# Kernel optimization log

Hardware: AMD Instinct MI355X
Metric: run time of the kernel (lower is better)

Reference implementation:

```python
import math
import jax, jax.numpy as jnp
import numpy as np
from jax import lax

# Block_mamba(dim=192): x = x + Mamba(LN1(x)); x = x + EinFFT(LN2(x), H, W)
DIM = 192
D_STATE = 64
D_CONV = 4
EXPAND = 2
D_INNER = EXPAND * DIM          # 384
DT_RANK = math.ceil(DIM / 16)   # 12
NUM_BLOCKS = 4                  # EinFFT hardcoded
BLOCK_SIZE = DIM // NUM_BLOCKS  # 48
LAMBDA = 0.01                   # softshrink threshold


def setup_inputs() -> dict:
    key = jax.random.key(0)
    ks = jax.random.split(key, 20)
    B, N, C = 4, 1024, DIM
    s = 0.02
    x = jax.random.normal(ks[0], (B, N, C), jnp.float32)
    inp = {
        "x": x,
        "ln1_w": jnp.ones((C,), jnp.float32),
        "ln1_b": jnp.zeros((C,), jnp.float32),
        "in_proj_w": jax.random.normal(ks[1], (2 * D_INNER, C), jnp.float32) * s,
        "conv_w": jax.random.normal(ks[2], (D_INNER, 1, D_CONV), jnp.float32) * 0.1,
        "conv_b": jnp.zeros((D_INNER,), jnp.float32),
        "x_proj_w": jax.random.normal(ks[3], (DT_RANK + 2 * D_STATE, D_INNER), jnp.float32) * s,
        "dt_proj_w": jax.random.normal(ks[4], (D_INNER, DT_RANK), jnp.float32) * (DT_RANK ** -0.5),
        "dt_proj_b": jax.random.uniform(ks[5], (D_INNER,), jnp.float32, -4.0, -2.0),
        "A_log": jnp.log(jnp.broadcast_to(jnp.arange(1, D_STATE + 1, dtype=jnp.float32), (D_INNER, D_STATE))),
        "D": jnp.ones((D_INNER,), jnp.float32),
        "out_proj_w": jax.random.normal(ks[6], (C, D_INNER), jnp.float32) * s,
        "ln2_w": jnp.ones((C,), jnp.float32),
        "ln2_b": jnp.zeros((C,), jnp.float32),
        "cw1": jax.random.normal(ks[7], (2, NUM_BLOCKS, BLOCK_SIZE, BLOCK_SIZE), jnp.float32) * s,
        "cw2": jax.random.normal(ks[8], (2, NUM_BLOCKS, BLOCK_SIZE, BLOCK_SIZE), jnp.float32) * s,
        "cb1": jax.random.normal(ks[9], (2, NUM_BLOCKS, BLOCK_SIZE), jnp.float32) * s,
        "cb2": jax.random.normal(ks[10], (2, NUM_BLOCKS, BLOCK_SIZE), jnp.float32) * s,
        "H": 32,
        "W": 32,
    }
    return inp


def layer_norm(x, w, b, eps=1e-5):
    mu = jnp.mean(x, axis=-1, keepdims=True)
    var = jnp.var(x, axis=-1, keepdims=True)
    return (x - mu) * lax.rsqrt(var + eps) * w + b


def mamba(x, in_proj_w, conv_w, conv_b, x_proj_w, dt_proj_w, dt_proj_b, A_log, D):
    B, L, C = x.shape
    xz = jnp.einsum('blc,ec->ble', x, in_proj_w)          # [B,L,2*D_INNER]
    xm, z = jnp.split(xz, 2, axis=-1)                      # each [B,L,D_INNER]
    # causal depthwise conv1d (torch pads both sides then slices [:, :, :L])
    xc = lax.conv_general_dilated(
        xm.transpose(0, 2, 1), conv_w, (1,), [(D_CONV - 1, 0)],
        dimension_numbers=('NCH', 'OIH', 'NCH'), feature_group_count=D_INNER)
    xm = jax.nn.silu(xc + conv_b[None, :, None]).transpose(0, 2, 1)  # [B,L,D_INNER]
    dbc = jnp.einsum('bld,ed->ble', xm, x_proj_w)
    dt, Bm, Cm = jnp.split(dbc, [DT_RANK, DT_RANK + D_STATE], axis=-1)
    delta = jax.nn.softplus(jnp.einsum('blr,dr->bld', dt, dt_proj_w) + dt_proj_b)  # [B,L,D_INNER]
    A = -jnp.exp(A_log)                                    # [D_INNER, D_STATE]

    def step(h, inp):
        d_t, B_t, C_t, x_t = inp                           # [B,d],[B,n],[B,n],[B,d]
        dA = jnp.exp(d_t[:, :, None] * A)                  # [B,d,n]
        h = h * dA + (d_t * x_t)[:, :, None] * B_t[:, None, :]
        y = jnp.einsum('bdn,bn->bd', h, C_t)
        return h, y

    h0 = jnp.zeros((B, D_INNER, D_STATE), x.dtype)
    xs = (delta.transpose(1, 0, 2), Bm.transpose(1, 0, 2), Cm.transpose(1, 0, 2), xm.transpose(1, 0, 2))
    _, ys = lax.scan(step, h0, xs)                         # ys: [L,B,d]
    y = ys.transpose(1, 0, 2) + xm * D
    y = y * jax.nn.silu(z)
    return jnp.einsum('bld,cd->blc', y, out_proj_w_global[0])


# small trick to keep mamba signature tidy
out_proj_w_global = [None]


def einfft(x, cw1, cw2, cb1, cb2):
    B, N, C = x.shape
    xv = x.reshape(B, N, NUM_BLOCKS, BLOCK_SIZE)
    pad1 = (1 << math.ceil(math.log2(N))) - N
    pad2 = (1 << math.ceil(math.log2(NUM_BLOCKS))) - NUM_BLOCKS
    if pad1 or pad2:
        xv = jnp.pad(xv, ((0, 0), (0, pad1), (0, pad2), (0, 0)))
    X = jnp.fft.fft2(xv, axes=(1, 2), norm='ortho')
    mul = lambda t, w: jnp.einsum('Bnbd,bdk->Bnbk', t, w)
    r1 = jax.nn.relu(mul(X.real, cw1[0]) - mul(X.imag, cw1[1]) + cb1[0])
    i1 = jax.nn.relu(mul(X.real, cw1[1]) + mul(X.imag, cw1[0]) + cb1[1])
    r2 = mul(r1, cw2[0]) - mul(i1, cw2[1]) + cb2[0]
    i2 = mul(r1, cw2[1]) + mul(i1, cw2[0]) + cb2[1]
    ss = lambda v: jnp.where(v > LAMBDA, v - LAMBDA, jnp.where(v < -LAMBDA, v + LAMBDA, jnp.zeros((), v.dtype)))
    Z = ss(r2) + 1j * ss(i2)
    y = jnp.fft.ifft2(Z, axes=(1, 2), norm='ortho')[:, :N, :NUM_BLOCKS, :]
    return y.real.reshape(B, N, C)  # torch .to(real dtype) keeps real part


def reference(x, ln1_w, ln1_b, in_proj_w, conv_w, conv_b, x_proj_w, dt_proj_w, dt_proj_b,
              A_log, D, out_proj_w, ln2_w, ln2_b, cw1, cw2, cb1, cb2, H, W):
    out_proj_w_global[0] = out_proj_w
    x = x + mamba(layer_norm(x, ln1_w, ln1_b), in_proj_w, conv_w, conv_b,
                  x_proj_w, dt_proj_w, dt_proj_b, A_log, D)
    x = x + einfft(layer_norm(x, ln2_w, ln2_b), cw1, cw2, cb1, cb2)
    return x
```

## Files before the change

kernel.cpp:

```cpp
#include <hip/hip_runtime.h>
#include <math.h>

#define PI_F 3.14159265358979323846f

typedef __attribute__((ext_vector_type(8))) short short8v;
typedef __attribute__((ext_vector_type(4))) float f32x4;

__device__ __forceinline__ float lane_bcast(float v, int l) {
  return __int_as_float(__builtin_amdgcn_readlane(__float_as_int(v), l));
}

__device__ __forceinline__ unsigned short f2bf(float f) {
  unsigned u = __float_as_uint(f);
  unsigned r = u + 0x7FFFu + ((u >> 16) & 1u);
  return (unsigned short)(r >> 16);
}

__device__ __forceinline__ float wave_reduce_sum(float v) {
  v += __shfl_xor(v, 32, 64);
  v += __shfl_xor(v, 16, 64);
  v += __shfl_xor(v, 8, 64);
  v += __shfl_xor(v, 4, 64);
  v += __shfl_xor(v, 2, 64);
  v += __shfl_xor(v, 1, 64);
  return v;
}

__global__ __launch_bounds__(256) void ln_kernel(const float* __restrict__ x,
    const float* __restrict__ w, const float* __restrict__ b,
    const float* __restrict__ ipw, unsigned short* __restrict__ obf,
    unsigned short* __restrict__ wbf) {
  int row = blockIdx.x * 4 + (threadIdx.x >> 6);
  int lane = threadIdx.x & 63;
  const float* xr = x + (size_t)row * 192;
  float v0 = xr[lane], v1 = xr[lane + 64], v2 = xr[lane + 128];
  float s  = wave_reduce_sum(v0 + v1 + v2);
  float s2 = wave_reduce_sum(v0 * v0 + v1 * v1 + v2 * v2);
  float mu  = s * (1.f / 192.f);
  float var = s2 * (1.f / 192.f) - mu * mu;
  float rs  = rsqrtf(var + 1e-5f);
  unsigned short* orow = obf + (size_t)row * 192;
  orow[lane]       = f2bf((v0 - mu) * rs * w[lane]       + b[lane]);
  orow[lane + 64]  = f2bf((v1 - mu) * rs * w[lane + 64]  + b[lane + 64]);
  orow[lane + 128] = f2bf((v2 - mu) * rs * w[lane + 128] + b[lane + 128]);
  for (int i = threadIdx.x; i < 144; i += 256) {
    int idx = blockIdx.x * 144 + i;
    wbf[idx] = f2bf(ipw[idx]);
  }
}

__global__ __launch_bounds__(256) void gemm_mfma_in(
    const unsigned short* __restrict__ Abf, const unsigned short* __restrict__ Wbf,
    float* __restrict__ C) {
  int wave = threadIdx.x >> 6;
  int lane = threadIdx.x & 63;
  int m0 = blockIdx.y * 64 + wave * 16;
  int n0 = blockIdx.x * 64;
  int rw = lane & 15;
  int g  = lane >> 4;
  const unsigned short* Ap = Abf + (size_t)(m0 + rw) * 192 + g * 8;
  const unsigned short* Wp = Wbf + (size_t)(n0 + rw) * 192 + g * 8;
  f32x4 acc[4];
#pragma unroll
  for (int f = 0; f < 4; ++f) acc[f] = (f32x4){0.f, 0.f, 0.f, 0.f};
#pragma unroll
  for (int kk = 0; kk < 192; kk += 32) {
    short8v a = *(const short8v*)(Ap + kk);
#pragma unroll
    for (int f = 0; f < 4; ++f) {
      short8v bfr = *(const short8v*)(Wp + (size_t)f * 16 * 192 + kk);
      acc[f] = __builtin_amdgcn_mfma_f32_16x16x32_bf16(a, bfr, acc[f], 0, 0, 0);
    }
  }
#pragma unroll
  for (int f = 0; f < 4; ++f)
#pragma unroll
    for (int r = 0; r < 4; ++r)
      C[(size_t)(m0 + g * 4 + r) * 768 + n0 + f * 16 + rw] = acc[f][r];
}

__global__ __launch_bounds__(256) void gemm_mfma_xp(
    const unsigned short* __restrict__ Abf, const unsigned short* __restrict__ Wbf,
    float* __restrict__ C) {
  int wave = threadIdx.x >> 6;
  int lane = threadIdx.x & 63;
  int m0 = blockIdx.y * 64 + wave * 16;
  int n0 = blockIdx.x * 64;
  int rw = lane & 15;
  int g  = lane >> 4;
  const unsigned short* Ap = Abf + (size_t)(m0 + rw) * 384 + g * 8;
  f32x4 acc[4];
#pragma unroll
  for (int f = 0; f < 4; ++f) acc[f] = (f32x4){0.f, 0.f, 0.f, 0.f};
  short8v bz = {0, 0, 0, 0, 0, 0, 0, 0};
#pragma unroll
  for (int kk = 0; kk < 384; kk += 32) {
    short8v a = *(const short8v*)(Ap + kk);
#pragma unroll
    for (int f = 0; f < 4; ++f) {
      int n = n0 + f * 16 + rw;
      short8v bfr = (n < 140)
        ? *(const short8v*)(Wbf + (size_t)n * 384 + g * 8 + kk) : bz;
      acc[f] = __builtin_amdgcn_mfma_f32_16x16x32_bf16(a, bfr, acc[f], 0, 0, 0);
    }
  }
#pragma unroll
  for (int f = 0; f < 4; ++f)
#pragma unroll
    for (int r = 0; r < 4; ++r) {
      int n = n0 + f * 16 + rw;
      if (n < 140)
        C[(size_t)(m0 + g * 4 + r) * 140 + n] = acc[f][r];
    }
}

__global__ __launch_bounds__(256) void gemm_at32m(const float* __restrict__ AT,
    const unsigned short* __restrict__ Wbf, const float* __restrict__ res,
    float* __restrict__ C) {
  __shared__ unsigned As[64][17];
  int tid = threadIdx.x;
  int wave = tid >> 6, lane = tid & 63;
  int n0 = blockIdx.x * 64;
  int m0 = blockIdx.y * 64;
  int bb = m0 >> 10;
  int t0 = m0 & 1023;
  const float* Ab = AT + ((size_t)bb * 384) * 1024 + t0;
  int col = tid & 63;
  int kq  = tid >> 6;
  int rw = lane & 15, g = lane >> 4;
  f32x4 acc[4];
#pragma unroll
  for (int f = 0; f < 4; ++f) acc[f] = (f32x4){0.f, 0.f, 0.f, 0.f};
#pragma unroll
  for (int kk = 0; kk < 384; kk += 32) {
#pragma unroll
    for (int p = 0; p < 4; ++p) {
      int k2 = kq + p * 4;
      int k = kk + k2 * 2;
      float f0 = Ab[(size_t)k * 1024 + col];
      float f1 = Ab[(size_t)(k + 1) * 1024 + col];
      As[col][k2] = (unsigned)f2bf(f0) | ((unsigned)f2bf(f1) << 16);
    }
    __syncthreads();
    int mrow = wave * 16 + rw;
    unsigned u0 = As[mrow][g * 4 + 0];
    unsigned u1 = As[mrow][g * 4 + 1];
    unsigned u2 = As[mrow][g * 4 + 2];
    unsigned u3 = As[mrow][g * 4 + 3];
    short8v a;
    ((unsigned*)&a)[0] = u0; ((unsigned*)&a)[1] = u1;
    ((unsigned*)&a)[2] = u2; ((unsigned*)&a)[3] = u3;
#pragma unroll
    for (int f = 0; f < 4; ++f) {
      short8v bfr = *(const short8v*)(Wbf + (size_t)(n0 + f * 16 + rw) * 384 + kk + g * 8);
      acc[f] = __builtin_amdgcn_mfma_f32_16x16x32_bf16(a, bfr, acc[f], 0, 0, 0);
    }
    __syncthreads();
  }
#pragma unroll
  for (int f = 0; f < 4; ++f)
#pragma unroll
    for (int r = 0; r < 4; ++r) {
      int m = m0 + wave * 16 + g * 4 + r;
      int n = n0 + f * 16 + rw;
      C[(size_t)m * 192 + n] = acc[f][r] + res[(size_t)m * 192 + n];
    }
}

__global__ __launch_bounds__(256) void ln2t_kernel(const float* __restrict__ x,
    const float* __restrict__ w, const float* __restrict__ b, float* __restrict__ xT) {
  __shared__ float xt[32][193];
  __shared__ float mu_s[32], rs_s[32];
  int blk = blockIdx.x;
  int Bi = blk >> 5;
  int t0 = (blk & 31) * 32;
  int tid = threadIdx.x;
  const float* xb = x + ((size_t)(Bi * 1024 + t0)) * 192;
  for (int i = tid; i < 32 * 192; i += 256) {
    xt[i / 192][i % 192] = xb[i];
  }
  __syncthreads();
  int row = tid >> 3, seg = tid & 7;
  float s = 0.f, s2 = 0.f;
  const float* xr = &xt[row][seg * 24];
#pragma unroll
  for (int k = 0; k < 24; ++k) { float v = xr[k]; s += v; s2 += v * v; }
  s  += __shfl_xor(s, 1, 64);  s  += __shfl_xor(s, 2, 64);  s  += __shfl_xor(s, 4, 64);
  s2 += __shfl_xor(s2, 1, 64); s2 += __shfl_xor(s2, 2, 64); s2 += __shfl_xor(s2, 4, 64);
  if (seg == 0) {
    float mu = s * (1.f / 192.f);
    float var = s2 * (1.f / 192.f) - mu * mu;
    mu_s[row] = mu;
    rs_s[row] = rsqrtf(var + 1e-5f);
  }
  __syncthreads();
  for (int i = tid; i < 32 * 192; i += 256) {
    int ch = i >> 5, r2 = i & 31;
    float v = (xt[r2][ch] - mu_s[r2]) * rs_s[r2] * w[ch] + b[ch];
    xT[((size_t)(Bi * 192 + ch)) * 1024 + t0 + r2] = v;
  }
}

__global__ __launch_bounds__(256) void conv_silu(const float* __restrict__ xz,
    const float* __restrict__ cw, const float* __restrict__ cb,
    float* __restrict__ xc, unsigned short* __restrict__ xcbf,
    const float* __restrict__ xpw, unsigned short* __restrict__ xpwbf) {
  if (threadIdx.x < 35) {
    int ci = blockIdx.x * 35 + threadIdx.x;
    xpwbf[ci] = f2bf(xpw[ci]);
  }
  int e4 = blockIdx.x * 256 + threadIdx.x;
  if (e4 >= 4 * 1024 * 96) return;
  int d4 = e4 % 96;
  int t  = (e4 / 96) % 1024;
  int b  = e4 / (96 * 1024);
  int d = d4 * 4;
  const float* base = xz + (size_t)(b * 1024) * 768 + d;
  float4 acc = *(const float4*)(cb + d);
  const float4* cwv = (const float4*)(cw + d * 4);
  float4 c0 = cwv[0], c1 = cwv[1], c2 = cwv[2], c3 = cwv[3];
#pragma unroll
  for (int j = 0; j < 4; ++j) {
    int tt = t - 3 + j;
    if (tt >= 0) {
      float4 v = *(const float4*)(base + (size_t)tt * 768);
      float w0 = (&c0.x)[j], w1 = (&c1.x)[j], w2 = (&c2.x)[j], w3 = (&c3.x)[j];
      acc.x = fmaf(v.x, w0, acc.x);
      acc.y = fmaf(v.y, w1, acc.y);
      acc.z = fmaf(v.z, w2, acc.z);
      acc.w = fmaf(v.w, w3, acc.w);
    }
  }
  float4 o;
  o.x = acc.x / (1.f + __expf(-acc.x));
  o.y = acc.y / (1.f + __expf(-acc.y));
  o.z = acc.z / (1.f + __expf(-acc.z));
  o.w = acc.w / (1.f + __expf(-acc.w));
  size_t idx = ((size_t)(b * 1024 + t) * 384) + d;
  *(float4*)(xc + idx) = o;
  uint2 pk;
  pk.x = (unsigned)f2bf(o.x) | ((unsigned)f2bf(o.y) << 16);
  pk.y = (unsigned)f2bf(o.z) | ((unsigned)f2bf(o.w) << 16);
  *(uint2*)(xcbf + idx) = pk;
}

__global__ __launch_bounds__(256) void delta_trans(const float* __restrict__ dbc,
    const float* __restrict__ dtw, const float* __restrict__ dtb,
    const float* __restrict__ xc, float* __restrict__ dltT, float* __restrict__ duT,
    const float* __restrict__ opw, unsigned short* __restrict__ opwbf) {
  __shared__ float dts[64][13];
  __shared__ float xt[64][65];
  int blk = blockIdx.x;
  int b  = blk / 96;
  int rem = blk % 96;
  int tt = rem / 6, dd = rem % 6;
  int t0 = tt * 64, d0 = dd * 64;
  int tid = threadIdx.x;
  for (int i = tid; i < 192; i += 256) {
    int idx = blk * 192 + i;
    opwbf[idx] = f2bf(opw[idx]);
  }
  for (int i = tid; i < 64 * 12; i += 256) {
    int tl = i / 12, r = i % 12;
    dts[tl][r] = dbc[((size_t)b * 1024 + t0 + tl) * 140 + r];
  }
  {
    int col = tid & 63, rg = tid >> 6;
#pragma unroll
    for (int j = 0; j < 16; ++j) {
      int row = j * 4 + rg;
      xt[row][col] = xc[((size_t)b * 1024 + t0 + row) * 384 + d0 + col];
    }
  }
  __syncthreads();
  int tl = tid & 63, grp = tid >> 6;
#pragma unroll
  for (int j = 0; j < 16; ++j) {
    int dl = grp * 16 + j;
    int d = d0 + dl;
    float s = dtb[d];
#pragma unroll
    for (int r = 0; r < 12; ++r) s += dts[tl][r] * dtw[d * 12 + r];
    float dlt = (s > 20.f) ? s : log1pf(__expf(s));
    size_t ob = ((size_t)b * 384 + d) * 1024 + t0 + tl;
    dltT[ob] = dlt;
    duT[ob]  = dlt * xt[tl][dl];
  }
}

#define SCAN_GBODY(G, BC, CC, XCV, ZVV, BN, CN, XCN, ZVN)                  \
  {                                                                        \
    int ts_ = (G) * 16;                                                    \
    if ((G) + 1 < 64) {                                                    \
      int tn_ = ts_ + 16;                                                  \
      _Pragma("unroll")                                                    \
      for (int i = 0; i < 16; ++i) {                                       \
        size_t ro = (size_t)(tn_ + i) * 140;                               \
        BN[i] = Bp[ro]; CN[i] = Cp[ro];                                    \
      }                                                                    \
      if (lane < 16) { XCN = xcp[(size_t)(tn_ + lane) * 384];              \
                       ZVN = xzp[(size_t)(tn_ + lane) * 768]; }            \
      if (((G) & 3) == 2) {                                                \
        int sn_ = ((G) >> 2) + 1;                                          \
        if (sn_ < 16) { dvN = dT[sn_ * 64 + lane];                         \
                        duN = uT[sn_ * 64 + lane]; }                       \
      }                                                                    \
    }                                                                      \
    int tb_ = ts_ & 63;                                                    \
    _Pragma("unroll")                                                      \
    for (int i = 0; i < 16; ++i) {                                         \
      float sdv = lane_bcast(dvC, tb_ + i);                                \
      float sdu = lane_bcast(duC, tb_ + i);                                \
      float a = exp2f(sdv * A);                                            \
      h = fmaf(h, a, sdu * BC[i]);                                         \
      tile[i][lane] = h * CC[i];                                           \
    }                                                                      \
    const float* trow_ = &tile[tq][q * 16];                                \
    float s_ = 0.f;                                                        \
    _Pragma("unroll")                                                      \
    for (int i = 0; i < 16; ++i) s_ += trow_[i];                           \
    s_ += __shfl_xor(s_, 16, 64);                                          \
    s_ += __shfl_xor(s_, 32, 64);                                          \
    if (lane < 16) {                                                       \
      float sg_ = ZVV / (1.f + __expf(-ZVV));                              \
      yp[ts_ + lane] = (s_ + XCV * ddv) * sg_;                             \
    }                                                                      \
    if (((G) & 3) == 3) { dvC = dvN; duC = duN; }                          \
  }

__global__ __launch_bounds__(64, 1) void scan_single(const float* __restrict__ dltT,
    const float* __restrict__ duT, const float* __restrict__ dbc,
    const float* __restrict__ A_log, const float* __restrict__ xc,
    const float* __restrict__ xz, const float* __restrict__ Dvec,
    float* __restrict__ yT) {
  __shared__ float tile[16][65];
  int bd = blockIdx.x;
  int b = bd / 384, d = bd % 384;
  int lane = threadIdx.x;
  float A = -__expf(A_log[d * 64 + lane]) * 1.44269504f;
  const float* dT = dltT + ((size_t)b * 384 + d) * 1024;
  const float* uT = duT  + ((size_t)b * 384 + d) * 1024;
  const float* Bp = dbc + ((size_t)b * 1024) * 140 + 12 + lane;
  const float* Cp = Bp + 64;
  float ddv = Dvec[d];
  float* yp = yT + ((size_t)b * 384 + d) * 1024;
  const float* xcp = xc + ((size_t)b * 1024) * 384 + d;
  const float* xzp = xz + ((size_t)b * 1024) * 768 + 384 + d;
  int tq = lane & 15;
  int q  = lane >> 4;
  float h = 0.f;

  float Ba[16], Ca[16], Bb[16], Cb[16];
  float dvC, duC, dvN = 0.f, duN = 0.f;
  float xcA = 0.f, zvA = 0.f, xcB = 0.f, zvB = 0.f;

  dvC = dT[lane];
  duC = uT[lane];
#pragma unroll
  for (int i = 0; i < 16; ++i) {
    size_t ro = (size_t)i * 140;
    Ba[i] = Bp[ro];
    Ca[i] = Cp[ro];
  }
  if (lane < 16) {
    xcA = xcp[(size_t)lane * 384];
    zvA = xzp[(size_t)lane * 768];
  }

  for (int gp = 0; gp < 32; ++gp) {
    int g0 = gp * 2;
    SCAN_GBODY(g0,     Ba, Ca, xcA, zvA, Bb, Cb, xcB, zvB)
    SCAN_GBODY(g0 + 1, Bb, Cb, xcB, zvB, Ba, Ca, xcA, zvA)
  }
}

__device__ __forceinline__ int rev4_10(int i) {
  unsigned r = __brev((unsigned)i) >> 22;
  return (int)(((r & 0x155u) << 1) | ((r >> 1) & 0x155u));
}

__device__ __forceinline__ void fft1024r4(float* __restrict__ re,
    float* __restrict__ im, const float* __restrict__ twc,
    const float* __restrict__ tws, int tid, float sgn) {
  for (int i = tid; i < 1024; i += 256) {
    int r = rev4_10(i);
    if (i < r) {
      float t = re[i]; re[i] = re[r]; re[r] = t;
      t = im[i]; im[i] = im[r]; im[r] = t;
    }
  }
  __syncthreads();
  {
    float4 ar = *(float4*)&re[tid * 4];
    float4 ai = *(float4*)&im[tid * 4];
    float apc_r = ar.x + ar.z, amc_r = ar.x - ar.z;
    float apc_i = ai.x + ai.z, amc_i = ai.x - ai.z;
    float bpd_r = ar.y + ar.w, bmd_r = ar.y - ar.w;
    float bpd_i = ai.y + ai.w, bmd_i = ai.y - ai.w;
    float4 yr, yi;
    yr.x = apc_r + bpd_r;        yi.x = apc_i + bpd_i;
    yr.z = apc_r - bpd_r;        yi.z = apc_i - bpd_i;
    yr.y = amc_r - sgn * bmd_i;  yi.y = amc_i + sgn * bmd_r;
    yr.w = amc_r + sgn * bmd_i;  yi.w = amc_i - sgn * bmd_r;
    *(float4*)&re[tid * 4] = yr;
    *(float4*)&im[tid * 4] = yi;
  }
  __syncthreads();
#pragma unroll
  for (int s = 1; s < 5; ++s) {
    int L = 1 << (2 * s);
    int tstep = 256 >> (2 * s);
    int j = tid & (L - 1);
    int base = ((tid >> (2 * s)) << (2 * s + 2)) + j;
    int i0 = base, i1 = base + L, i2 = base + 2 * L, i3 = base + 3 * L;
    int x1i = j * tstep;
    float w1c = twc[x1i],     w1s = tws[x1i];
    float w2c = twc[2 * x1i], w2s = tws[2 * x1i];
    float w3c = twc[3 * x1i], w3s = tws[3 * x1i];
    float ar_ = re[i0], ai_ = im[i0];
    float br_ = re[i1], bi_ = im[i1];
    float cr_ = re[i2], ci_ = im[i2];
    float dr_ = re[i3], di_ = im[i3];
    float tbr = br_ * w1c - bi_ * w1s, tbi = br_ * w1s + bi_ * w1c;
    float tcr = cr_ * w2c - ci_ * w2s, tci = cr_ * w2s + ci_ * w2c;
    float tdr = dr_ * w3c - di_ * w3s, tdi = dr_ * w3s + di_ * w3c;
    float apc_r = ar_ + tcr, amc_r = ar_ - tcr;
    float apc_i = ai_ + tci, amc_i = ai_ - tci;
    float bpd_r = tbr + tdr, bmd_r = tbr - tdr;
    float bpd_i = tbi + tdi, bmd_i = tbi - tdi;
    re[i0] = apc_r + bpd_r;       im[i0] = apc_i + bpd_i;
    re[i2] = apc_r - bpd_r;       im[i2] = apc_i - bpd_i;
    re[i1] = amc_r - sgn * bmd_i; im[i1] = amc_i + sgn * bmd_r;
    re[i3] = amc_r + sgn * bmd_i; im[i3] = amc_i - sgn * bmd_r;
    __syncthreads();
  }
}

__global__ __launch_bounds__(256) void fft_fwd(const float* __restrict__ x2T,
    float* __restrict__ Xre, float* __restrict__ Xim) {
  __shared__ float re[1024];
  __shared__ float im[1024];
  __shared__ float twc[768];
  __shared__ float tws[768];
  int blk = blockIdx.x;
  int c = blk & 3;
  int rest = blk >> 2;
  int d = rest % 48, Bi = rest / 48;
  int tid = threadIdx.x;
  for (int k = tid; k < 768; k += 256) {
    float sv, cv;
    __sincosf(-PI_F * (float)k * (1.f / 512.f), &sv, &cv);
    twc[k] = cv; tws[k] = sv;
  }
  const float* pb = x2T + ((size_t)(Bi * 192 + d)) * 1024;
  for (int n = tid; n < 1024; n += 256) {
    float v0 = pb[n];
    float v1 = pb[48 * 1024 + n];
    float v2 = pb[96 * 1024 + n];
    float v3 = pb[144 * 1024 + n];
    float rr, ii;
    if (c == 0)      { rr = v0 + v1 + v2 + v3; ii = 0.f; }
    else if (c == 1) { rr = v0 - v2;           ii = -(v1 - v3); }
    else if (c == 2) { rr = v0 - v1 + v2 - v3; ii = 0.f; }
    else             { rr = v0 - v2;           ii = (v1 - v3); }
    re[n] = rr; im[n] = ii;
  }
  __syncthreads();
  fft1024r4(re, im, twc, tws, tid, -1.0f);
  float* xo_r = Xre + ((size_t)((Bi * 4 + c) * 48 + d)) * 1024;
  float* xo_i = Xim + ((size_t)((Bi * 4 + c) * 48 + d)) * 1024;
  for (int k = tid; k < 1024; k += 256) {
    xo_r[k] = re[k] * (1.f / 64.f);
    xo_i[k] = im[k] * (1.f / 64.f);
  }
}

__global__ __launch_bounds__(256) void mix_fused(float* __restrict__ Xre,
    float* __restrict__ Xim, const float* __restrict__ cw1,
    const float* __restrict__ cw2, const float* __restrict__ cb1,
    const float* __restrict__ cb2) {
  __shared__ float r1s[4][48][4];
  __shared__ float i1s[4][48][4];
  int w = threadIdx.x >> 6;
  int j = threadIdx.x & 63;
  int rg = blockIdx.x * 4 + w;
  int kq = rg & 255;
  int b  = (rg >> 8) & 3;
  int Bi = rg >> 10;
  int k0 = kq * 4;
  size_t xbase = ((size_t)((Bi * 4 + b) * 48)) * 1024 + k0;
  if (j < 48) {
    const float* wr = cw1 + b * 2304;
    const float* wi = cw1 + 9216 + b * 2304;
    float b1r = cb1[b * 48 + j], b1i = cb1[192 + b * 48 + j];
    float ar[4] = {b1r, b1r, b1r, b1r};
    float ai[4] = {b1i, b1i, b1i, b1i};
#pragma unroll 8
    for (int dd = 0; dd < 48; ++dd) {
      float4 xr = *(const float4*)(Xre + xbase + (size_t)dd * 1024);
      float4 xi = *(const float4*)(Xim + xbase + (size_t)dd * 1024);
      float wrv = wr[dd * 48 + j], wiv = wi[dd * 48 + j];
      ar[0] = fmaf(xr.x, wrv, ar[0]); ar[0] = fmaf(-xi.x, wiv, ar[0]);
      ai[0] = fmaf(xr.x, wiv, ai[0]); ai[0] = fmaf(xi.x, wrv, ai[0]);
      ar[1] = fmaf(xr.y, wrv, ar[1]); ar[1] = fmaf(-xi.y, wiv, ar[1]);
      ai[1] = fmaf(xr.y, wiv, ai[1]); ai[1] = fmaf(xi.y, wrv, ai[1]);
      ar[2] = fmaf(xr.z, wrv, ar[2]); ar[2] = fmaf(-xi.z, wiv, ar[2]);
      ai[2] = fmaf(xr.z, wiv, ai[2]); ai[2] = fmaf(xi.z, wrv, ai[2]);
      ar[3] = fmaf(xr.w, wrv, ar[3]); ar[3] = fmaf(-xi.w, wiv, ar[3]);
      ai[3] = fmaf(xr.w, wiv, ai[3]); ai[3] = fmaf(xi.w, wrv, ai[3]);
    }
    float4 r1v, i1v;
    r1v.x = fmaxf(ar[0], 0.f); r1v.y = fmaxf(ar[1], 0.f);
    r1v.z = fmaxf(ar[2], 0.f); r1v.w = fmaxf(ar[3], 0.f);
    i1v.x = fmaxf(ai[0], 0.f); i1v.y = fmaxf(ai[1], 0.f);
    i1v.z = fmaxf(ai[2], 0.f); i1v.w = fmaxf(ai[3], 0.f);
    *(float4*)&r1s[w][j][0] = r1v;
    *(float4*)&i1s[w][j][0] = i1v;
    const float* wr2 = cw2 + b * 2304;
    const float* wi2 = cw2 + 9216 + b * 2304;
    float b2r = cb2[b * 48 + j], b2i = cb2[192 + b * 48 + j];
    float a2r[4] = {b2r, b2r, b2r, b2r};
    float a2i[4] = {b2i, b2i, b2i, b2i};
#pragma unroll 8
    for (int dd = 0; dd < 48; ++dd) {
      float4 rv = *(const float4*)&r1s[w][dd][0];
      float4 iv = *(const float4*)&i1s[w][dd][0];
      float wrv = wr2[dd * 48 + j], wiv = wi2[dd * 48 + j];
      a2r[0] = fmaf(rv.x, wrv, a2r[0]); a2r[0] = fmaf(-iv.x, wiv, a2r[0]);
      a2i[0] = fmaf(rv.x, wiv, a2i[0]); a2i[0] = fmaf(iv.x, wrv, a2i[0]);
      a2r[1] = fmaf(rv.y, wrv, a2r[1]); a2r[1] = fmaf(-iv.y, wiv, a2r[1]);
      a2i[1] = fmaf(rv.y, wiv, a2i[1]); a2i[1] = fmaf(iv.y, wrv, a2i[1]);
      a2r[2] = fmaf(rv.z, wrv, a2r[2]); a2r[2] = fmaf(-iv.z, wiv, a2r[2]);
      a2i[2] = fmaf(rv.z, wiv, a2i[2]); a2i[2] = fmaf(iv.z, wrv, a2i[2]);
      a2r[3] = fmaf(rv.w, wrv, a2r[3]); a2r[3] = fmaf(-iv.w, wiv, a2r[3]);
      a2i[3] = fmaf(rv.w, wiv, a2i[3]); a2i[3] = fmaf(iv.w, wrv, a2i[3]);
    }
    float4 zr, zi;
#pragma unroll
    for (int r = 0; r < 4; ++r) {
      float vr = a2r[r], vi = a2i[r];
      (&zr.x)[r] = (vr > 0.01f) ? vr - 0.01f : ((vr < -0.01f) ? vr + 0.01f : 0.f);
      (&zi.x)[r] = (vi > 0.01f) ? vi - 0.01f : ((vi < -0.01f) ? vi + 0.01f : 0.f);
    }
    size_t obase = ((size_t)((Bi * 4 + b) * 48 + j)) * 1024 + k0;
    *(float4*)(Xre + obase) = zr;
    *(float4*)(Xim + obase) = zi;
  }
}

__global__ __launch_bounds__(256) void fft_inv(const float* __restrict__ Zre,
    const float* __restrict__ Zim, const float* __restrict__ x1, float* __restrict__ out) {
  __shared__ float re[1024];
  __shared__ float im[1024];
  __shared__ float twc[768];
  __shared__ float tws[768];
  int blk = blockIdx.x;
  int c = blk & 3;
  int rest = blk >> 2;
  int d = rest % 48, Bi = rest / 48;
  int tid = threadIdx.x;
  for (int k = tid; k < 768; k += 256) {
    float sv, cv;
    __sincosf(PI_F * (float)k * (1.f / 512.f), &sv, &cv);
    twc[k] = cv; tws[k] = sv;
  }
  const float* zr0 = Zre + ((size_t)((Bi * 4) * 48 + d)) * 1024;
  const float* zi0 = Zim + ((size_t)((Bi * 4) * 48 + d)) * 1024;
  const int cs = 48 * 1024;
  for (int k = tid; k < 1024; k += 256) {
    float r0 = zr0[k], r1v = zr0[cs + k], r2 = zr0[2 * cs + k], r3 = zr0[3 * cs + k];
    float i0 = zi0[k], i1v = zi0[cs + k], i2 = zi0[2 * cs + k], i3 = zi0[3 * cs + k];
    float rr, ii;
    if (c == 0)      { rr = r0 + r1v + r2 + r3;  ii = i0 + i1v + i2 + i3; }
    else if (c == 1) { rr = r0 - i1v - r2 + i3;  ii = i0 + r1v - i2 - r3; }
    else if (c == 2) { rr = r0 - r1v + r2 - r3;  ii = i0 - i1v + i2 - i3; }
    else             { rr = r0 + i1v - r2 - i3;  ii = i0 - r1v - i2 + r3; }
    re[k] = rr; im[k] = ii;
  }
  __syncthreads();
  fft1024r4(re, im, twc, tws, tid, 1.0f);
  for (int n = tid; n < 1024; n += 256) {
    size_t o = (size_t)(Bi * 1024 + n) * 192 + c * 48 + d;
    out[o] = x1[o] + re[n] * (1.f / 64.f);
  }
}

extern "C" void kernel_launch(void* const* d_in, const int* in_sizes, int n_in,
                              void* d_out, int out_size, void* d_ws, size_t ws_size,
                              hipStream_t stream) {
  const float* x         = (const float*)d_in[0];
  const float* ln1_w     = (const float*)d_in[1];
  const float* ln1_b     = (const float*)d_in[2];
  const float* in_proj_w = (const float*)d_in[3];
  const float* conv_w    = (const float*)d_in[4];
  const float* conv_b    = (const float*)d_in[5];
  const float* x_proj_w  = (const float*)d_in[6];
  const float* dt_proj_w = (const float*)d_in[7];
  const float* dt_proj_b = (const float*)d_in[8];
  const float* A_log     = (const float*)d_in[9];
  const float* Dvec      = (const float*)d_in[10];
  const float* out_proj_w= (const float*)d_in[11];
  const float* ln2_w     = (const float*)d_in[12];
  const float* ln2_b     = (const float*)d_in[13];
  const float* cw1       = (const float*)d_in[14];
  const float* cw2       = (const float*)d_in[15];
  const float* cb1       = (const float*)d_in[16];
  const float* cb2       = (const float*)d_in[17];
  float* out = (float*)d_out;
  float* ws  = (float*)d_ws;

  float* xz   = ws;
  float* xc   = xz  + 3145728;
  float* dbc  = xc  + 1572864;
  float* dltT = dbc + 573440;
  float* yvT  = dltT + 1572864;
  float* xln  = yvT + 1572864;
  float* x2T  = xln + 786432;
  float* Xre  = x2T + 786432;
  float* Xim  = Xre + 786432;
  float* duT = Xre;
  float* x1 = xln;
  unsigned short* xbf = (unsigned short*)(Xim + 786432);
  unsigned short* wbf = (unsigned short*)(Xim + 786432 + 393216);
  unsigned short* opwbf = (unsigned short*)(Xim + 786432 + 393216 + 36864);
  unsigned short* xcbf  = (unsigned short*)xln;
  unsigned short* xpwbf = (unsigned short*)x2T;

  ln_kernel<<<1024, 256, 0, stream>>>(x, ln1_w, ln1_b, in_proj_w, xbf, wbf);
  gemm_mfma_in<<<dim3(12, 64), 256, 0, stream>>>(xbf, wbf, xz);
  conv_silu<<<1536, 256, 0, stream>>>(xz, conv_w, conv_b, xc, xcbf, x_proj_w, xpwbf);
  gemm_mfma_xp<<<dim3(3, 64), 256, 0, stream>>>(xcbf, xpwbf, dbc);
  delta_trans<<<384, 256, 0, stream>>>(dbc, dt_proj_w, dt_proj_b, xc, dltT, duT,
                                       out_proj_w, opwbf);
  scan_single<<<1536, 64, 0, stream>>>(dltT, duT, dbc, A_log, xc, xz, Dvec, yvT);
  gemm_at32m<<<dim3(3, 64), 256, 0, stream>>>(yvT, opwbf, x, x1);
  ln2t_kernel<<<128, 256, 0, stream>>>(x1, ln2_w, ln2_b, x2T);
  fft_fwd<<<768, 256, 0, stream>>>(x2T, Xre, Xim);
  mix_fused<<<1024, 256, 0, stream>>>(Xre, Xim, cw1, cw2, cb1, cb2);
  fft_inv<<<768, 256, 0, stream>>>(Xre, Xim, x1, out);
}
```

Measured before the change: 296.7 us.

## Share B/C state tiles across six channels per block in selective scan

The scan kernel now runs 384 threads per block, six waves each handling one channel of the same batch. The B and C state vectors are staged cooperatively into double-buffered shared memory and reused by all six channels, so each channel no longer reloads them from global memory. In exchange the kernel adds a block-wide barrier per 16-step group and launches only 256 blocks, which lowers parallelism on a large GPU.

```diff
diff --git a/kernel.cpp b/kernel.cpp
--- a/kernel.cpp
+++ b/kernel.cpp
@@ -288,89 +288,106 @@
   }
 }
 
-#define SCAN_GBODY(G, BC, CC, XCV, ZVV, BN, CN, XCN, ZVN)                  \
-  {                                                                        \
-    int ts_ = (G) * 16;                                                    \
-    if ((G) + 1 < 64) {                                                    \
-      int tn_ = ts_ + 16;                                                  \
-      _Pragma("unroll")                                                    \
-      for (int i = 0; i < 16; ++i) {                                       \
-        size_t ro = (size_t)(tn_ + i) * 140;                               \
-        BN[i] = Bp[ro]; CN[i] = Cp[ro];                                    \
-      }                                                                    \
-      if (lane < 16) { XCN = xcp[(size_t)(tn_ + lane) * 384];              \
-                       ZVN = xzp[(size_t)(tn_ + lane) * 768]; }            \
-      if (((G) & 3) == 2) {                                                \
-        int sn_ = ((G) >> 2) + 1;                                          \
-        if (sn_ < 16) { dvN = dT[sn_ * 64 + lane];                         \
-                        duN = uT[sn_ * 64 + lane]; }                       \
-      }                                                                    \
-    }                                                                      \
-    int tb_ = ts_ & 63;                                                    \
-    _Pragma("unroll")                                                      \
-    for (int i = 0; i < 16; ++i) {                                         \
-      float sdv = lane_bcast(dvC, tb_ + i);                                \
-      float sdu = lane_bcast(duC, tb_ + i);                                \
-      float a = exp2f(sdv * A);                                            \
-      h = fmaf(h, a, sdu * BC[i]);                                         \
-      tile[i][lane] = h * CC[i];                                           \
-    }                                                                      \
-    const float* trow_ = &tile[tq][q * 16];                                \
-    float s_ = 0.f;                                                        \
-    _Pragma("unroll")                                                      \
-    for (int i = 0; i < 16; ++i) s_ += trow_[i];                           \
-    s_ += __shfl_xor(s_, 16, 64);                                          \
-    s_ += __shfl_xor(s_, 32, 64);                                          \
-    if (lane < 16) {                                                       \
-      float sg_ = ZVV / (1.f + __expf(-ZVV));                              \
-      yp[ts_ + lane] = (s_ + XCV * ddv) * sg_;                             \
-    }                                                                      \
-    if (((G) & 3) == 3) { dvC = dvN; duC = duN; }                          \
-  }
-
-__global__ __launch_bounds__(64, 1) void scan_single(const float* __restrict__ dltT,
+__global__ __launch_bounds__(384, 1) void scan_shared(const float* __restrict__ dltT,
     const float* __restrict__ duT, const float* __restrict__ dbc,
     const float* __restrict__ A_log, const float* __restrict__ xc,
     const float* __restrict__ xz, const float* __restrict__ Dvec,
     float* __restrict__ yT) {
-  __shared__ float tile[16][65];
-  int bd = blockIdx.x;
-  int b = bd / 384, d = bd % 384;
-  int lane = threadIdx.x;
+  __shared__ float Bs[2][16][64];
+  __shared__ float Cs[2][16][64];
+  __shared__ float tile[6][16][65];
+  int blk = blockIdx.x;
+  int b = blk >> 6;
+  int d0 = (blk & 63) * 6;
+  int tid = threadIdx.x;
+  int w = tid >> 6;
+  int lane = tid & 63;
+  int d = d0 + w;
   float A = -__expf(A_log[d * 64 + lane]) * 1.44269504f;
   const float* dT = dltT + ((size_t)b * 384 + d) * 1024;
   const float* uT = duT  + ((size_t)b * 384 + d) * 1024;
-  const float* Bp = dbc + ((size_t)b * 1024) * 140 + 12 + lane;
-  const float* Cp = Bp + 64;
+  const float* Bg = dbc + (size_t)(b * 1024) * 140 + 12;
   float ddv = Dvec[d];
   float* yp = yT + ((size_t)b * 384 + d) * 1024;
-  const float* xcp = xc + ((size_t)b * 1024) * 384 + d;
-  const float* xzp = xz + ((size_t)b * 1024) * 768 + 384 + d;
-  int tq = lane & 15;
-  int q  = lane >> 4;
+  const float* xcp = xc + (size_t)(b * 1024) * 384 + d;
+  const float* xzp = xz + (size_t)(b * 1024) * 768 + 384 + d;
+  int tq = lane & 15, q = lane >> 4;
+  int i0 = tid, i1 = tid + 384, i2 = tid + 768;
+  size_t o0 = (size_t)(i0 >> 6) * 140 + (i0 & 63);
+  size_t o1 = (size_t)(i1 >> 6) * 140 + (i1 & 63);
+  size_t o2 = (size_t)(i2 >> 6) * 140 + (i2 & 63);
+  bool has2 = (i2 < 1024);
+
+  {
+    float b0 = Bg[o0], c0 = Bg[o0 + 64];
+    float b1 = Bg[o1], c1 = Bg[o1 + 64];
+    float b2 = 0.f, c2 = 0.f;
+    if (has2) { b2 = Bg[o2]; c2 = Bg[o2 + 64]; }
+    Bs[0][i0 >> 6][i0 & 63] = b0;  Cs[0][i0 >> 6][i0 & 63] = c0;
+    Bs[0][i1 >> 6][i1 & 63] = b1;  Cs[0][i1 >> 6][i1 & 63] = c1;
+    if (has2) { Bs[0][i2 >> 6][i2 & 63] = b2;  Cs[0][i2 >> 6][i2 & 63] = c2; }
+  }
   float h = 0.f;
-
-  float Ba[16], Ca[16], Bb[16], Cb[16];
-  float dvC, duC, dvN = 0.f, duN = 0.f;
-  float xcA = 0.f, zvA = 0.f, xcB = 0.f, zvB = 0.f;
-
-  dvC = dT[lane];
-  duC = uT[lane];
-#pragma unroll
-  for (int i = 0; i < 16; ++i) {
-    size_t ro = (size_t)i * 140;
-    Ba[i] = Bp[ro];
-    Ca[i] = Cp[ro];
-  }
+  float dv64 = dT[lane], du64 = uT[lane];
+  float xcv = 0.f, zv = 0.f;
   if (lane < 16) {
-    xcA = xcp[(size_t)lane * 384];
-    zvA = xzp[(size_t)lane * 768];
-  }
-
-  for (int gp = 0; gp < 32; ++gp) {
-    int g0 = gp * 2;
-    SCAN_GBODY(g0,     Ba, Ca, xcA, zvA, Bb, Cb, xcB, zvB)
-    SCAN_GBODY(g0 + 1, Bb, Cb, xcB, zvB, Ba, Ca, xcA, zvA)
+    xcv = xcp[(size_t)lane * 384];
+    zv  = xzp[(size_t)lane * 768];
+  }
+  __syncthreads();
+
+  for (int g = 0; g < 64; ++g) {
+    int cur = g & 1, nxt = cur ^ 1;
+    if (g + 1 < 64) {
+      const float* Bg1 = Bg + (size_t)(g + 1) * (16 * 140);
+      float b0 = Bg1[o0], c0 = Bg1[o0 + 64];
+      float b1 = Bg1[o1], c1 = Bg1[o1 + 64];
+      float b2 = 0.f, c2 = 0.f;
+      if (has2) { b2 = Bg1[o2]; c2 = Bg1[o2 + 64]; }
+      Bs[nxt][i0 >> 6][i0 & 63] = b0;  Cs[nxt][i0 >> 6][i0 & 63] = c0;
+      Bs[nxt][i1 >> 6][i1 & 63] = b1;  Cs[nxt][i1 >> 6][i1 & 63] = c1;
+      if (has2) { Bs[nxt][i2 >> 6][i2 & 63] = b2;  Cs[nxt][i2 >> 6][i2 & 63] = c2; }
+    }
+    float xcvN = 0.f, zvN = 0.f, dvN = dv64, duN = du64;
+    if (g + 1 < 64) {
+      int ts1 = (g + 1) * 16;
+      if (lane < 16) {
+        xcvN = xcp[(size_t)(ts1 + lane) * 384];
+        zvN  = xzp[(size_t)(ts1 + lane) * 768];
+      }
+      if (((g + 1) & 3) == 0) {
+        int sg = (g + 1) >> 2;
+        dvN = dT[sg * 64 + lane];
+        duN = uT[sg * 64 + lane];
+      }
+    }
+    int tb = (g & 3) * 16;
+    float Bv[16], Cv[16];
+#pragma unroll
+    for (int i = 0; i < 16; ++i) {
+      Bv[i] = Bs[cur][i][lane];
+      Cv[i] = Cs[cur][i][lane];
+    }
+#pragma unroll
+    for (int i = 0; i < 16; ++i) {
+      float sdv = lane_bcast(dv64, tb + i);
+      float sdu = lane_bcast(du64, tb + i);
+      float a = exp2f(sdv * A);
+      h = fmaf(h, a, sdu * Bv[i]);
+      tile[w][i][lane] = h * Cv[i];
+    }
+    const float* trow = &tile[w][tq][q * 16];
+    float s_ = 0.f;
+#pragma unroll
+    for (int i = 0; i < 16; ++i) s_ += trow[i];
+    s_ += __shfl_xor(s_, 16, 64);
+    s_ += __shfl_xor(s_, 32, 64);
+    if (lane < 16) {
+      float sg2 = zv / (1.f + __expf(-zv));
+      yp[g * 16 + lane] = (s_ + xcv * ddv) * sg2;
+    }
+    xcv = xcvN; zv = zvN; dv64 = dvN; du64 = duN;
+    __syncthreads();
   }
 }
 
@@ -632,7 +649,7 @@
   gemm_mfma_xp<<<dim3(3, 64), 256, 0, stream>>>(xcbf, xpwbf, dbc);
   delta_trans<<<384, 256, 0, stream>>>(dbc, dt_proj_w, dt_proj_b, xc, dltT, duT,
                                        out_proj_w, opwbf);
-  scan_single<<<1536, 64, 0, stream>>>(dltT, duT, dbc, A_log, xc, xz, Dvec, yvT);
+  scan_shared<<<256, 384, 0, stream>>>(dltT, duT, dbc, A_log, xc, xz, Dvec, yvT);
   gemm_at32m<<<dim3(3, 64), 256, 0, stream>>>(yvT, opwbf, x, x1);
   ln2t_kernel<<<128, 256, 0, stream>>>(x1, ln2_w, ln2_b, x2T);
   fft_fwd<<<768, 256, 0, stream>>>(x2T, Xre, Xim);
```

Result: slower. 318.0 us (+7.2%).
